# Kernel optimization log

Hardware: AMD Instinct MI355X
Metric: run time of the kernel (lower is better)

The kernel has to match this reference:

```python
import jax, jax.numpy as jnp
import numpy as np
import math

B, S, D = 1, 4096, 2048
H, KVH, HD = 16, 4, 128
ROPE_THETA = 10000.0


def _rope_tables(seq_len, head_dim, theta):
    inv_freq = 1.0 / (theta ** (jnp.arange(0, head_dim, 2, dtype=jnp.float32) / head_dim))
    t = jnp.arange(seq_len, dtype=jnp.float32)
    freqs = jnp.outer(t, inv_freq)                      # [S, HD/2]
    emb = jnp.concatenate([freqs, freqs], axis=-1)      # [S, HD]
    return jnp.cos(emb)[None, None], jnp.sin(emb)[None, None]  # [1,1,S,HD]


def setup_inputs() -> dict:
    key = jax.random.key(0)
    ks = jax.random.split(key, 8)
    hidden_states = jax.random.normal(ks[0], (B, S, D), dtype=jnp.float32)
    # additive causal mask [B,1,S,S]
    neg = jnp.finfo(jnp.float32).min
    causal = jnp.where(jnp.tril(jnp.ones((S, S), dtype=bool)), 0.0, neg)
    attention_mask = jnp.broadcast_to(causal[None, None], (B, 1, S, S)).astype(jnp.float32)
    cos, sin = _rope_tables(S, HD, ROPE_THETA)
    gate = jax.random.uniform(ks[1], (B, S), dtype=jnp.float32, minval=0.05, maxval=1.0)
    sc = lambda fan_in: 1.0 / math.sqrt(fan_in)
    Wq = jax.random.normal(ks[2], (D, H * HD), dtype=jnp.float32) * sc(D)
    Wk = jax.random.normal(ks[3], (D, KVH * HD), dtype=jnp.float32) * sc(D)
    Wv = jax.random.normal(ks[4], (D, KVH * HD), dtype=jnp.float32) * sc(D)
    Wo = jax.random.normal(ks[5], (H * HD, D), dtype=jnp.float32) * sc(H * HD)
    return {"hidden_states": hidden_states, "attention_mask": attention_mask,
            "cos": cos, "sin": sin, "gate": gate,
            "Wq": Wq, "Wk": Wk, "Wv": Wv, "Wo": Wo}


def _rotate_half(x):
    h = x.shape[-1] // 2
    return jnp.concatenate([-x[..., h:], x[..., :h]], axis=-1)


def reference(hidden_states, attention_mask, cos, sin, gate, Wq, Wk, Wv, Wo):
    bsz, q_len, _ = hidden_states.shape
    # projections -> [B, heads, S, HD]
    q = (hidden_states @ Wq).reshape(bsz, q_len, H, HD).transpose(0, 2, 1, 3)
    k = (hidden_states @ Wk).reshape(bsz, q_len, KVH, HD).transpose(0, 2, 1, 3)
    v = (hidden_states @ Wv).reshape(bsz, q_len, KVH, HD).transpose(0, 2, 1, 3)
    # inline RoPE
    q = q * cos + _rotate_half(q) * sin
    k = k * cos + _rotate_half(k) * sin
    # GQA: repeat-interleave kv heads to match q heads
    g = H // KVH
    k = jnp.repeat(k, g, axis=1)
    v = jnp.repeat(v, g, axis=1)
    scores = jnp.einsum('bhqd,bhkd->bhqk', q, k) / math.sqrt(HD)
    scores = scores + attention_mask
    scores = scores + jnp.log(gate + 1e-8)[:, None, None, :]  # gate over kv positions
    weights = jax.nn.softmax(scores.astype(jnp.float32), axis=-1).astype(q.dtype)
    out = jnp.einsum('bhqk,bhkd->bhqd', weights, v)
    out = out.transpose(0, 2, 1, 3).reshape(bsz, q_len, H * HD)
    return out @ Wo
```

## Files before the change

kernel.cpp:

```cpp
#include <hip/hip_runtime.h>
#include <math.h>

#define S_LEN 4096
#define DMODEL 2048
#define NH 16
#define NKVH 4
#define HD 128
#define LDQKV 3072

typedef __attribute__((ext_vector_type(4))) float f32x4;
typedef __attribute__((ext_vector_type(8))) short bf16x8;
typedef __attribute__((ext_vector_type(4))) unsigned short us4;

static __device__ __forceinline__ unsigned short f2bf(float f) {
  unsigned int u = __builtin_bit_cast(unsigned int, f);
  u += 0x7fffu + ((u >> 16) & 1u);
  return (unsigned short)(u >> 16);
}
static __device__ __forceinline__ float bf2f(unsigned short h) {
  unsigned int u = ((unsigned int)h) << 16;
  return __builtin_bit_cast(float, u);
}
static __device__ __forceinline__ unsigned int cvt_pk_bf16(float lo, float hi) {
  unsigned int r;
  asm("v_cvt_pk_bf16_f32 %0, %1, %2" : "=v"(r) : "v"(lo), "v"(hi));
  return r;
}

#define GLDS16(g, l) __builtin_amdgcn_global_load_lds( \
    (__attribute__((address_space(1))) void*)(g), \
    (__attribute__((address_space(3))) void*)(l), 16, 0, 0)


__global__ __launch_bounds__(256) void k_prep(
    const float* __restrict__ hid, unsigned short* __restrict__ Xb,
    const float* __restrict__ Wq, const float* __restrict__ Wk,
    const float* __restrict__ Wv, const float* __restrict__ Wo,
    unsigned short* __restrict__ Wt, unsigned short* __restrict__ Wot) {
  __shared__ float tile[64][65];
  const int b = blockIdx.x, t = threadIdx.x;
  if (b < 8192) {
    int i = b * 256 + t;
    const float4* s = (const float4*)hid;
    float4 v = s[i];
    us4 o = { f2bf(v.x), f2bf(v.y), f2bf(v.z), f2bf(v.w) };
    *(us4*)(Xb + (size_t)i * 4) = o;
    return;
  }
  const int bb = b - 8192;
  const float* src;
  unsigned short* dst;
  int N, c;
  if (bb < 1024)      { src = Wq; dst = Wt;                       N = 2048; c = bb; }
  else if (bb < 1280) { src = Wk; dst = Wt + (size_t)2048 * 2048; N = 512;  c = bb - 1024; }
  else if (bb < 1536) { src = Wv; dst = Wt + (size_t)2560 * 2048; N = 512;  c = bb - 1280; }
  else                { src = Wo; dst = Wot;                      N = 2048; c = bb - 1536; }
  const int k0 = (c & 31) * 64, n0 = (c >> 5) * 64;
#pragma unroll
  for (int i = 0; i < 16; ++i) {
    int idx = t + i * 256;
    int r = idx >> 6, cc = idx & 63;
    tile[r][cc] = src[(size_t)(k0 + r) * N + n0 + cc];
  }
  __syncthreads();
#pragma unroll
  for (int i = 0; i < 16; ++i) {
    int idx = t + i * 256;
    int r = idx >> 6, cc = idx & 63;
    dst[(size_t)(n0 + r) * 2048 + k0 + cc] = f2bf(tile[cc][r]);
  }
}


__global__ __launch_bounds__(256) void k_vt(
    const unsigned short* __restrict__ QKV, unsigned short* __restrict__ Vt) {
  __shared__ unsigned short tile[64][72];
  const int b = blockIdx.x, t = threadIdx.x;
  const int s0 = (b & 63) * 64, c0 = (b >> 6) * 64;
#pragma unroll
  for (int i = 0; i < 16; ++i) {
    int idx = t + i * 256;
    int r = idx >> 6, cc = idx & 63;
    tile[r][cc] = QKV[(size_t)(s0 + r) * LDQKV + DMODEL + NKVH * HD + c0 + cc];
  }
  __syncthreads();
#pragma unroll
  for (int i = 0; i < 16; ++i) {
    int idx = t + i * 256;
    int r = idx >> 6, cc = idx & 63;
    int pc = (cc & 3) * 16 + (cc >> 2);
    Vt[(size_t)(c0 + r) * S_LEN + s0 + cc] = tile[pc][r];
  }
}


template<int MODE>
__global__ __launch_bounds__(256) void k_gemm_bt(
    const unsigned short* __restrict__ A, const unsigned short* __restrict__ Bt,
    void* __restrict__ Cp, int M, int N, int K,
    const float* __restrict__ cp, const float* __restrict__ sp) {
  __shared__ __attribute__((aligned(16))) unsigned short As[128 * 32];
  __shared__ __attribute__((aligned(16))) unsigned short Bs[128 * 32];
  const int t = threadIdx.x;
  const int wave = t >> 6, lane = t & 63;
  const int lr = lane & 15, lg = lane >> 4;
  const int bm = blockIdx.x * 128, bn = blockIdx.y * 128;
  const int wr = wave * 32;
  f32x4 acc[2][8];
#pragma unroll
  for (int i = 0; i < 2; ++i)
#pragma unroll
    for (int j = 0; j < 8; ++j) acc[i][j] = (f32x4){0.f, 0.f, 0.f, 0.f};

  for (int k0 = 0; k0 < K; k0 += 32) {
    __syncthreads();
#pragma unroll
    for (int i = 0; i < 2; ++i) {
      const int cb = (wave * 2 + i) * 64;
      const int c = cb + lane;
      const int row = c >> 2, kc = c & 3;
      const int ksw = (kc ^ (row & 3)) * 8;
      GLDS16(A + (size_t)(bm + row) * K + k0 + ksw, (char*)As + cb * 16);
      GLDS16(Bt + (size_t)(bn + row) * K + k0 + ksw, (char*)Bs + cb * 16);
    }
    asm volatile("s_waitcnt vmcnt(0)" ::: "memory");
    __syncthreads();
    bf16x8 af[2], bfr[8];
#pragma unroll
    for (int mi = 0; mi < 2; ++mi) {
      const int row = wr + mi * 16 + lr;
      af[mi] = *(const bf16x8*)(As + row * 32 + ((lg ^ (lr & 3)) * 8));
    }
#pragma unroll
    for (int ni = 0; ni < 8; ++ni) {
      const int row = ni * 16 + lr;
      bfr[ni] = *(const bf16x8*)(Bs + row * 32 + ((lg ^ (lr & 3)) * 8));
    }
#pragma unroll
    for (int mi = 0; mi < 2; ++mi)
#pragma unroll
      for (int ni = 0; ni < 8; ++ni)
        acc[mi][ni] = __builtin_amdgcn_mfma_f32_16x16x32_bf16(af[mi], bfr[ni], acc[mi][ni], 0, 0, 0);
  }

  if (MODE == 1 && bn < NKVH * HD + DMODEL) {
    const float qs = bn < DMODEL ? 0.12751589341664477f : 1.0f;
    unsigned short* o = (unsigned short*)Cp;
#pragma unroll
    for (int mi = 0; mi < 2; ++mi)
#pragma unroll
      for (int r = 0; r < 4; ++r) {
        const int m = bm + wr + mi * 16 + lg * 4 + r;
#pragma unroll
        for (int ni = 0; ni < 4; ++ni) {
          const int d = ni * 16 + lr;
          const float c = cp[m * HD + d], s = sp[m * HD + d];
          const float x1 = acc[mi][ni][r], x2 = acc[mi][ni + 4][r];
          o[(size_t)m * N + bn + d]      = f2bf((x1 * c - x2 * s) * qs);
          o[(size_t)m * N + bn + d + 64] = f2bf((x2 * c + x1 * s) * qs);
        }
      }
    return;
  }
#pragma unroll
  for (int mi = 0; mi < 2; ++mi)
#pragma unroll
    for (int ni = 0; ni < 8; ++ni)
#pragma unroll
      for (int r = 0; r < 4; ++r) {
        const int m = bm + wr + mi * 16 + lg * 4 + r;
        const int n = bn + ni * 16 + lr;
        if (MODE == 2) ((float*)Cp)[(size_t)m * N + n] = acc[mi][ni][r];
        else ((unsigned short*)Cp)[(size_t)m * N + n] = f2bf(acc[mi][ni][r]);
      }
}


#define STAGE_KV(kt_, buf_) do { \
  const int kv0_ = (kt_) * 64; \
  _Pragma("unroll") \
  for (int i_ = 0; i_ < 2; ++i_) { \
    const int cb_ = (wave * 2 + i_) * 64; \
    const int c_ = cb_ + lane; \
    { const int row_ = c_ >> 4, kc_ = c_ & 15; \
      GLDS16(Kp + (size_t)(kv0_ + row_) * LDQKV + ((kc_ ^ (row_ & 7)) * 8), \
             (char*)Ks[buf_] + cb_ * 16); } \
    { const int d_ = c_ >> 3, kc_ = c_ & 7; \
      GLDS16(Vp + (size_t)d_ * S_LEN + kv0_ + ((kc_ ^ (d_ & 7)) * 8), \
             (char*)Vs[buf_] + cb_ * 16); } \
  } \
} while (0)

__global__ __launch_bounds__(512) void k_attn(
    const unsigned short* __restrict__ QKV, const unsigned short* __restrict__ Vt,
    const float* __restrict__ gate, unsigned short* __restrict__ Oattn) {
  __shared__ __attribute__((aligned(16))) unsigned short Ks[2][64 * 128];
  __shared__ __attribute__((aligned(16))) unsigned short Vs[2][128 * 64];
  __shared__ __attribute__((aligned(16))) unsigned short Ps[8][2][16][72];
  const int st = blockIdx.x, h = blockIdx.y, kvh = h >> 2;
  const int t = threadIdx.x, wave = t >> 6, lane = t & 63;
  const int lr = lane & 15, lg = lane >> 4;
  const unsigned short* Qp = QKV + h * HD;
  const unsigned short* Kp = QKV + DMODEL + kvh * HD;
  const unsigned short* Vp = Vt + (size_t)kvh * HD * S_LEN;
  bf16x8 vb_ones;
  {
    const short one = (short)0x3F80, z = 0;
    const short e = (lr == 0) ? one : z;
    vb_ones = (bf16x8){e, e, e, e, e, e, e, e};
  }

  const int q0 = st * 256;
  const int nt = 4 * st + 4;
  const int qb[2] = { q0 + wave * 32 + lg * 4, q0 + wave * 32 + 16 + lg * 4 };

  bf16x8 qf[2][4];
#pragma unroll
  for (int g = 0; g < 2; ++g) {
    const size_t qoff = (size_t)(q0 + wave * 32 + g * 16 + lr) * LDQKV;
#pragma unroll
    for (int ks = 0; ks < 4; ++ks)
      qf[g][ks] = *(const bf16x8*)(Qp + qoff + ks * 32 + lg * 8);
  }
  f32x4 acc[2][8];
#pragma unroll
  for (int g = 0; g < 2; ++g)
#pragma unroll
    for (int j = 0; j < 8; ++j) acc[g][j] = (f32x4){0.f, 0.f, 0.f, 0.f};
  f32x4 acc_s[2] = { (f32x4){0.f, 0.f, 0.f, 0.f}, (f32x4){0.f, 0.f, 0.f, 0.f} };
  float mrow[2][4] = { {-3e38f, -3e38f, -3e38f, -3e38f}, {-3e38f, -3e38f, -3e38f, -3e38f} };
  f32x4 sc[2][4];
  float g4[4];

  STAGE_KV(0, 0);

  for (int kt = 0; kt < nt; ++kt) {
    const int kv0 = kt * 64;
    if (kt + 1 < nt) {
      STAGE_KV(kt + 1, (kt + 1) & 1);
      asm volatile("s_waitcnt vmcnt(4)" ::: "memory");
    } else {
      asm volatile("s_waitcnt vmcnt(0)" ::: "memory");
    }
    __builtin_amdgcn_s_barrier();
    const unsigned short* Kb = Ks[kt & 1];
    const unsigned short* Vb = Vs[kt & 1];
#pragma unroll
    for (int cf = 0; cf < 4; ++cf) g4[cf] = gate[kv0 + cf * 16 + lr];

    __builtin_amdgcn_s_setprio(1);
#pragma unroll
    for (int cf = 0; cf < 4; ++cf) {
      sc[0][cf] = (f32x4){0.f, 0.f, 0.f, 0.f};
      sc[1][cf] = (f32x4){0.f, 0.f, 0.f, 0.f};
      const int row = cf * 16 + lr;
#pragma unroll
      for (int ks = 0; ks < 4; ++ks) {
        bf16x8 kb = *(const bf16x8*)(Kb + row * 128 + (((ks * 4 + lg) ^ (lr & 7)) * 8));
        sc[0][cf] = __builtin_amdgcn_mfma_f32_16x16x32_bf16(qf[0][ks], kb, sc[0][cf], 0, 0, 0);
        sc[1][cf] = __builtin_amdgcn_mfma_f32_16x16x32_bf16(qf[1][ks], kb, sc[1][cf], 0, 0, 0);
      }
    }
    __builtin_amdgcn_s_setprio(0);

    const bool tail = kv0 >= q0;
#pragma unroll
    for (int g = 0; g < 2; ++g) {
      if (tail) {
#pragma unroll
        for (int cf = 0; cf < 4; ++cf) {
          const int kpos = kv0 + cf * 16 + lr;
#pragma unroll
          for (int r = 0; r < 4; ++r)
            sc[g][cf][r] = (kpos <= qb[g] + r) ? sc[g][cf][r] : -3e38f;
        }
      }
      float lmax[4];
#pragma unroll
      for (int r = 0; r < 4; ++r)
        lmax[r] = fmaxf(fmaxf(sc[g][0][r], sc[g][1][r]), fmaxf(sc[g][2][r], sc[g][3][r]));
      bool need = (lmax[0] > mrow[g][0] + 11.5416f) | (lmax[1] > mrow[g][1] + 11.5416f) |
                  (lmax[2] > mrow[g][2] + 11.5416f) | (lmax[3] > mrow[g][3] + 11.5416f);
      if (__any(need)) {
        float tm[4] = {lmax[0], lmax[1], lmax[2], lmax[3]};
#pragma unroll
        for (int off = 8; off; off >>= 1)
#pragma unroll
          for (int r = 0; r < 4; ++r) tm[r] = fmaxf(tm[r], __shfl_xor(tm[r], off));
#pragma unroll
        for (int r = 0; r < 4; ++r) {
          const float mn = fmaxf(mrow[g][r], tm[r]);
          const float alpha = __builtin_amdgcn_exp2f(mrow[g][r] - mn);
          mrow[g][r] = mn;
#pragma unroll
          for (int j = 0; j < 8; ++j) acc[g][j][r] *= alpha;
          acc_s[g][r] *= alpha;
        }
      }
#pragma unroll
      for (int r = 0; r < 4; ++r) {
        float p0 = __builtin_amdgcn_exp2f(sc[g][0][r] - mrow[g][r]) * g4[0];
        float p1 = __builtin_amdgcn_exp2f(sc[g][1][r] - mrow[g][r]) * g4[1];
        float p2 = __builtin_amdgcn_exp2f(sc[g][2][r] - mrow[g][r]) * g4[2];
        float p3 = __builtin_amdgcn_exp2f(sc[g][3][r] - mrow[g][r]) * g4[3];
        uint2 pk = { cvt_pk_bf16(p0, p1), cvt_pk_bf16(p2, p3) };
        *(uint2*)(&Ps[wave][g][lg * 4 + r][lr * 4]) = pk;
      }
    }
    __builtin_amdgcn_s_setprio(1);
#pragma unroll
    for (int ks = 0; ks < 2; ++ks) {
      bf16x8 pa0 = *(const bf16x8*)(&Ps[wave][0][lr][ks * 32 + lg * 8]);
      bf16x8 pa1 = *(const bf16x8*)(&Ps[wave][1][lr][ks * 32 + lg * 8]);
#pragma unroll
      for (int j = 0; j < 8; ++j) {
        const int d = j * 16 + lr;
        bf16x8 vb = *(const bf16x8*)(Vb + d * 64 + (((ks * 4 + lg) ^ (lr & 7)) * 8));
        acc[0][j] = __builtin_amdgcn_mfma_f32_16x16x32_bf16(pa0, vb, acc[0][j], 0, 0, 0);
        acc[1][j] = __builtin_amdgcn_mfma_f32_16x16x32_bf16(pa1, vb, acc[1][j], 0, 0, 0);
      }
      acc_s[0] = __builtin_amdgcn_mfma_f32_16x16x32_bf16(pa0, vb_ones, acc_s[0], 0, 0, 0);
      acc_s[1] = __builtin_amdgcn_mfma_f32_16x16x32_bf16(pa1, vb_ones, acc_s[1], 0, 0, 0);
    }
    __builtin_amdgcn_s_setprio(0);
    __builtin_amdgcn_s_barrier();
  }

#pragma unroll
  for (int g = 0; g < 2; ++g) {
    float inv[4];
#pragma unroll
    for (int r = 0; r < 4; ++r)
      inv[r] = 1.0f / __shfl(acc_s[g][r], lane & 48);
#pragma unroll
    for (int j = 0; j < 8; ++j)
#pragma unroll
      for (int r = 0; r < 4; ++r)
        Oattn[(size_t)(qb[g] + r) * DMODEL + h * HD + j * 16 + lr] = f2bf(acc[g][j][r] * inv[r]);
  }
}


extern "C" void kernel_launch(void* const* d_in, const int* in_sizes, int n_in,
                              void* d_out, int out_size, void* d_ws, size_t ws_size,
                              hipStream_t stream) {
  (void)in_sizes; (void)n_in; (void)out_size; (void)ws_size;
  const float* hid  = (const float*)d_in[0];
  const float* cosp = (const float*)d_in[2];
  const float* sinp = (const float*)d_in[3];
  const float* gate = (const float*)d_in[4];
  const float* Wq   = (const float*)d_in[5];
  const float* Wk   = (const float*)d_in[6];
  const float* Wv   = (const float*)d_in[7];
  const float* Wo   = (const float*)d_in[8];
  float* out = (float*)d_out;
  char* ws = (char*)d_ws;
  unsigned short* Xb   = (unsigned short*)(ws);
  unsigned short* Wt   = (unsigned short*)(ws + (size_t)16777216);
  unsigned short* Wot  = (unsigned short*)(ws + (size_t)29360128);
  unsigned short* QKV  = (unsigned short*)(ws + (size_t)37748736);
  unsigned short* Oatt = (unsigned short*)(ws + (size_t)62914560);
  unsigned short* Vt   = (unsigned short*)(ws + (size_t)79691776);

  k_prep<<<10752, 256, 0, stream>>>(hid, Xb, Wq, Wk, Wv, Wo, Wt, Wot);
  k_gemm_bt<1><<<dim3(32, 24), 256, 0, stream>>>(Xb, Wt, QKV, 4096, 3072, 2048, cosp, sinp);
  k_vt<<<512, 256, 0, stream>>>(QKV, Vt);
  k_attn<<<dim3(16, 16), 512, 0, stream>>>(QKV, Vt, gate, Oatt);
  k_gemm_bt<2><<<dim3(32, 16), 256, 0, stream>>>(Oatt, Wot, out, 4096, 2048, 2048, nullptr, nullptr);
}
```

Before: 303.4 us.

## Split attention KV range into two chunks and merge with a combine kernel

The attention kernel now gives each query tile two blocks, each covering half of its causal KV tiles. Each block writes unnormalized bf16 partial outputs plus its row max and row sum, and a new combine kernel merges them with log-sum-exp weights. Blocks are launched heaviest-first, giving 512 blocks instead of 256 to fill more CUs and even out the causal load imbalance. The cost is an extra kernel launch, extra global traffic for the partials, and a bf16 rounding of the unnormalized partials; scratch buffers reuse the already-consumed Xb and Wt regions.

```diff
diff --git a/kernel.cpp b/kernel.cpp
--- a/kernel.cpp
+++ b/kernel.cpp
@@ -10,6 +10,7 @@
 
 typedef __attribute__((ext_vector_type(4))) float f32x4;
 typedef __attribute__((ext_vector_type(8))) short bf16x8;
+typedef __attribute__((ext_vector_type(8))) unsigned short us8;
 typedef __attribute__((ext_vector_type(4))) unsigned short us4;
 
 static __device__ __forceinline__ unsigned short f2bf(float f) {
@@ -193,11 +194,16 @@
 
 __global__ __launch_bounds__(512) void k_attn(
     const unsigned short* __restrict__ QKV, const unsigned short* __restrict__ Vt,
-    const float* __restrict__ gate, unsigned short* __restrict__ Oattn) {
+    const float* __restrict__ gate, unsigned short* __restrict__ N1,
+    unsigned short* __restrict__ N2, float2* __restrict__ Ms) {
   __shared__ __attribute__((aligned(16))) unsigned short Ks[2][64 * 128];
   __shared__ __attribute__((aligned(16))) unsigned short Vs[2][128 * 64];
   __shared__ __attribute__((aligned(16))) unsigned short Ps[8][2][16][72];
-  const int st = blockIdx.x, h = blockIdx.y, kvh = h >> 2;
+  const int bx = blockIdx.x;
+  const int st = 15 - (bx >> 5);
+  const int rem = bx & 31;
+  const int h = rem >> 1, chunk = rem & 1;
+  const int kvh = h >> 2;
   const int t = threadIdx.x, wave = t >> 6, lane = t & 63;
   const int lr = lane & 15, lg = lane >> 4;
   const unsigned short* Qp = QKV + h * HD;
@@ -211,7 +217,8 @@
   }
 
   const int q0 = st * 256;
-  const int nt = 4 * st + 4;
+  const int half_nt = 2 * st + 2;
+  const int kt_lo = chunk * half_nt, kt_hi = kt_lo + half_nt;
   const int qb[2] = { q0 + wave * 32 + lg * 4, q0 + wave * 32 + 16 + lg * 4 };
 
   bf16x8 qf[2][4];
@@ -232,11 +239,11 @@
   f32x4 sc[2][4];
   float g4[4];
 
-  STAGE_KV(0, 0);
-
-  for (int kt = 0; kt < nt; ++kt) {
+  STAGE_KV(kt_lo, kt_lo & 1);
+
+  for (int kt = kt_lo; kt < kt_hi; ++kt) {
     const int kv0 = kt * 64;
-    if (kt + 1 < nt) {
+    if (kt + 1 < kt_hi) {
       STAGE_KV(kt + 1, (kt + 1) & 1);
       asm volatile("s_waitcnt vmcnt(4)" ::: "memory");
     } else {
@@ -326,18 +333,47 @@
     __builtin_amdgcn_s_barrier();
   }
 
+  unsigned short* Nd = chunk ? N2 : N1;
 #pragma unroll
   for (int g = 0; g < 2; ++g) {
-    float inv[4];
-#pragma unroll
-    for (int r = 0; r < 4; ++r)
-      inv[r] = 1.0f / __shfl(acc_s[g][r], lane & 48);
 #pragma unroll
     for (int j = 0; j < 8; ++j)
 #pragma unroll
       for (int r = 0; r < 4; ++r)
-        Oattn[(size_t)(qb[g] + r) * DMODEL + h * HD + j * 16 + lr] = f2bf(acc[g][j][r] * inv[r]);
-  }
+        Nd[(size_t)(qb[g] + r) * DMODEL + h * HD + j * 16 + lr] = f2bf(acc[g][j][r]);
+  }
+  if (lr == 0) {
+#pragma unroll
+    for (int g = 0; g < 2; ++g)
+#pragma unroll
+      for (int r = 0; r < 4; ++r)
+        Ms[(size_t)(chunk * 16 + h) * S_LEN + qb[g] + r] =
+            make_float2(mrow[g][r], acc_s[g][r]);
+  }
+}
+
+
+__global__ __launch_bounds__(256) void k_comb(
+    unsigned short* __restrict__ N1, const unsigned short* __restrict__ N2,
+    const float2* __restrict__ Ms) {
+  const int gid = blockIdx.x * 256 + threadIdx.x;
+  const size_t e = (size_t)gid * 8;
+  const int row = (int)(e >> 11);
+  const int col = (int)(e & 2047);
+  const int h = col >> 7;
+  const float2 a = Ms[(size_t)h * S_LEN + row];
+  const float2 b = Ms[(size_t)(16 + h) * S_LEN + row];
+  const float m = fmaxf(a.x, b.x);
+  const float w1 = __builtin_amdgcn_exp2f(a.x - m);
+  const float w2 = __builtin_amdgcn_exp2f(b.x - m);
+  const float inv = 1.0f / (w1 * a.y + w2 * b.y);
+  us8 n1 = *(const us8*)(N1 + e);
+  us8 n2 = *(const us8*)(N2 + e);
+  us8 o;
+#pragma unroll
+  for (int k = 0; k < 8; ++k)
+    o[k] = f2bf((w1 * bf2f(n1[k]) + w2 * bf2f(n2[k])) * inv);
+  *(us8*)(N1 + e) = o;
 }
 
 
@@ -361,10 +397,13 @@
   unsigned short* QKV  = (unsigned short*)(ws + (size_t)37748736);
   unsigned short* Oatt = (unsigned short*)(ws + (size_t)62914560);
   unsigned short* Vt   = (unsigned short*)(ws + (size_t)79691776);
+  unsigned short* Np   = Xb;
+  float2* Ms           = (float2*)Wt;
 
   k_prep<<<10752, 256, 0, stream>>>(hid, Xb, Wq, Wk, Wv, Wo, Wt, Wot);
   k_gemm_bt<1><<<dim3(32, 24), 256, 0, stream>>>(Xb, Wt, QKV, 4096, 3072, 2048, cosp, sinp);
   k_vt<<<512, 256, 0, stream>>>(QKV, Vt);
-  k_attn<<<dim3(16, 16), 512, 0, stream>>>(QKV, Vt, gate, Oatt);
+  k_attn<<<512, 512, 0, stream>>>(QKV, Vt, gate, Oatt, Np, Ms);
+  k_comb<<<4096, 256, 0, stream>>>(Oatt, Np, Ms);
   k_gemm_bt<2><<<dim3(32, 16), 256, 0, stream>>>(Oatt, Wot, out, 4096, 2048, 2048, nullptr, nullptr);
 }
```

New measurement: 247.1 us (median of 2 runs). -18.6%, faster.
